# Kernel optimization log

Hardware: AMD Instinct MI355X
Metric: run time of the kernel (lower is better)

## Reference

```python
import jax, jax.numpy as jnp
import numpy as np

N = 4096
IN_DIM, HID, OUT_DIM = 512, 256, 64
PROP_STEP = 10
LAM_HAT = 0.9
SCAD_A = 3.7
EPS = 1e-8


def setup_inputs() -> dict:
    key = jax.random.key(0)
    kA, kF, k1, k2 = jax.random.split(key, 4)
    # sparse symmetric 0/1 adjacency, zero diagonal (add_loops adds I later)
    u = jax.random.uniform(kA, (N, N), dtype=jnp.float32)
    A = (u < 0.005).astype(jnp.float32)
    A = jnp.maximum(A, A.T)
    A = A * (1.0 - jnp.eye(N, dtype=jnp.float32))
    F = jax.random.normal(kF, (N, IN_DIM), dtype=jnp.float32)
    W1 = jax.random.normal(k1, (IN_DIM, HID), dtype=jnp.float32) / np.sqrt(IN_DIM)
    b1 = jnp.zeros((HID,), dtype=jnp.float32)
    W2 = jax.random.normal(k2, (HID, OUT_DIM), dtype=jnp.float32) / np.sqrt(HID)
    b2 = jnp.zeros((OUT_DIM,), dtype=jnp.float32)
    raw_gamma = jnp.zeros((PROP_STEP,), dtype=jnp.float32)
    return {"A": A, "F": F, "W1": W1, "b1": b1, "W2": W2, "b2": b2,
            "raw_gamma": raw_gamma}


def reference(A, F, W1, b1, W2, b2, raw_gamma):
    lam = 1.0 / LAM_HAT - 1.0
    a = SCAD_A
    # MLP (dropout inactive at inference)
    F0 = jax.nn.relu(F @ W1 + b1) @ W2 + b2            # [N, out_dim]
    eye = jnp.eye(A.shape[0], dtype=A.dtype)
    A = A + eye                                        # add_loops
    D = A.sum(-1)                                      # [N]
    D_sq = jnp.sqrt(D)[:, None]                        # [N, 1]
    A_tilde = A / D_sq / D_sq.T                        # sym_norm: D^-1/2 A D^-1/2
    gammas = jax.nn.sigmoid(raw_gamma) * 2.0           # per-layer gamma in (0, 2)

    def step(Fc, gamma_k):
        Fn = Fc / D_sq
        nrm = jnp.linalg.norm(Fn, axis=-1, keepdims=True)
        Fu = Fn / jnp.maximum(nrm, 1e-12)
        # cosine distance in [0, 2]; detached as in torch (.detach())
        y = jax.lax.stop_gradient(1.0 - Fu @ Fu.T)     # [N, N]
        lam_k = jnp.maximum(gamma_k / a, EPS)
        t = a * lam_k
        safe_y = jnp.where(y <= 0.0, 1.0, y)
        w_mid = (t - y) / ((a - 1.0) * safe_y)
        # SCAD weight: 1 for y<=lam_k, linear decay on [lam_k, a*lam_k], 0 beyond
        W = jnp.where(y <= lam_k, 1.0, jnp.where(y <= t, w_mid, 0.0))
        W = W * (1.0 - eye)
        W = jnp.where(jnp.isnan(W), 1.0, W)
        Q_hat = ((W * A).sum(-1) / D + lam)[:, None]   # [N, 1]
        F_new = (W * A_tilde) @ Fc / Q_hat + lam * F0 / Q_hat
        return F_new, None

    F_out, _ = jax.lax.scan(step, F0, gammas)
    return F_out
```

## Files before the change

kernel.cpp:

```cpp
#include <hip/hip_runtime.h>
#include <hip/hip_bf16.h>

#define N_NODES 4096
#define IN_DIM  512
#define HID_DIM 256
#define OUT_DIM 64
#define PROP_STEP 10
#define MAX_DEG 128
#define KSPLIT  4
#define MLP1_BLOCKS (64 * 4 * KSPLIT)
#define LAM_CONST (1.0f/0.9f - 1.0f)
#define SCAD_A 3.7f

__device__ __forceinline__ ushort f2bf(float f) {
    unsigned u = __float_as_uint(f);
    unsigned r = (u + 0x7FFFu + ((u >> 16) & 1u)) >> 16;
    return (ushort)r;
}
__device__ __forceinline__ unsigned pack2(float lo, float hi) {
    return (unsigned)f2bf(lo) | ((unsigned)f2bf(hi) << 16);
}
__device__ __forceinline__ float bflo(unsigned u) { return __uint_as_float(u << 16); }
__device__ __forceinline__ float bfhi(unsigned u) { return __uint_as_float(u & 0xFFFF0000u); }

__device__ __forceinline__ float wave_reduce_add(float v) {
#pragma unroll
    for (int off = 32; off > 0; off >>= 1) v += __shfl_xor(v, off, 64);
    return v;
}

__global__ __launch_bounds__(256) void build_mlp1(
    const float* __restrict__ A, const float* __restrict__ F,
    const float* __restrict__ W1, float* __restrict__ Hp,
    int* __restrict__ ell, int* __restrict__ deg,
    float* __restrict__ invD, float* __restrict__ invDsq)
{
    if (blockIdx.x < MLP1_BLOCKS) {
        __shared__ float sA[16][68];
        __shared__ float sB[16][68];
        int bid = blockIdx.x;
        int t  = threadIdx.x;
        int m0 = (bid & 63) * 64;
        int n0 = ((bid >> 6) & 3) * 64;
        int kp = bid >> 8;
        int tm = (t & 15) * 4;
        int tn = (t >> 4) * 4;
        int ar = t >> 2;
        int ac = (t & 3) * 4;
        int br = t >> 4;
        int bc = (t & 15) * 4;
        float acc[4][4] = {};
        int k0 = kp * (IN_DIM / KSPLIT);
        for (int kc = k0; kc < k0 + IN_DIM / KSPLIT; kc += 16) {
            float4 va = *(const float4*)(F  + (size_t)(m0 + ar) * IN_DIM + kc + ac);
            float4 vb = *(const float4*)(W1 + (size_t)(kc + br) * HID_DIM + n0 + bc);
            __syncthreads();
            sA[ac + 0][ar] = va.x;
            sA[ac + 1][ar] = va.y;
            sA[ac + 2][ar] = va.z;
            sA[ac + 3][ar] = va.w;
            *(float4*)&sB[br][bc] = vb;
            __syncthreads();
#pragma unroll
            for (int k = 0; k < 16; k++) {
                float4 a = *(const float4*)&sA[k][tm];
                float4 b = *(const float4*)&sB[k][tn];
                acc[0][0] += a.x * b.x; acc[0][1] += a.x * b.y; acc[0][2] += a.x * b.z; acc[0][3] += a.x * b.w;
                acc[1][0] += a.y * b.x; acc[1][1] += a.y * b.y; acc[1][2] += a.y * b.z; acc[1][3] += a.y * b.w;
                acc[2][0] += a.z * b.x; acc[2][1] += a.z * b.y; acc[2][2] += a.z * b.z; acc[2][3] += a.z * b.w;
                acc[3][0] += a.w * b.x; acc[3][1] += a.w * b.y; acc[3][2] += a.w * b.z; acc[3][3] += a.w * b.w;
            }
        }
        float* Hb = Hp + (size_t)kp * N_NODES * HID_DIM;
#pragma unroll
        for (int r = 0; r < 4; r++) {
            *(float4*)&Hb[(size_t)(m0 + tm + r) * HID_DIM + n0 + tn] =
                make_float4(acc[r][0], acc[r][1], acc[r][2], acc[r][3]);
        }
    } else {
        __shared__ int cnt;
        int i = blockIdx.x - MLP1_BLOCKS;
        int t = threadIdx.x;
        if (t == 0) cnt = 0;
        __syncthreads();
        const float4* row = (const float4*)(A + (size_t)i * N_NODES);
        for (int q = t; q < N_NODES / 4; q += 256) {
            float4 v = row[q];
            if (v.x != 0.0f) { int p = atomicAdd(&cnt, 1); if (p < MAX_DEG) ell[i * MAX_DEG + p] = q * 4 + 0; }
            if (v.y != 0.0f) { int p = atomicAdd(&cnt, 1); if (p < MAX_DEG) ell[i * MAX_DEG + p] = q * 4 + 1; }
            if (v.z != 0.0f) { int p = atomicAdd(&cnt, 1); if (p < MAX_DEG) ell[i * MAX_DEG + p] = q * 4 + 2; }
            if (v.w != 0.0f) { int p = atomicAdd(&cnt, 1); if (p < MAX_DEG) ell[i * MAX_DEG + p] = q * 4 + 3; }
        }
        __syncthreads();
        if (t == 0) {
            int c = cnt;
            if (c > MAX_DEG) c = MAX_DEG;
            deg[i] = c;
            int pad = (c + 15) & ~15;
            if (pad > MAX_DEG) pad = MAX_DEG;
            for (int p = c; p < pad; p++) ell[i * MAX_DEG + p] = i;
            float d = (float)(cnt + 1);
            invD[i] = 1.0f / d;
            invDsq[i] = rsqrtf(d);
        }
    }
}

__global__ __launch_bounds__(256) void mlp2r(
    const float* __restrict__ Hp, const float* __restrict__ b1,
    const float* __restrict__ W2, const float* __restrict__ b2,
    const float* __restrict__ invDsq,
    float* __restrict__ F0, unsigned* __restrict__ P0, float* __restrict__ nrm0)
{
    __shared__ float sW2[HID_DIM * OUT_DIM];
    __shared__ float hbuf[4][HID_DIM];
    int tid  = threadIdx.x;
    int wid  = tid >> 6, lane = tid & 63;
    int row  = blockIdx.x * 4 + wid;
    const size_t PS = (size_t)N_NODES * HID_DIM;

    for (int i = tid; i < HID_DIM * OUT_DIM / 4; i += 256)
        ((float4*)sW2)[i] = ((const float4*)W2)[i];

    const float* hrow = Hp + (size_t)row * HID_DIM + lane * 4;
    float4 s0 = *(const float4*)(hrow);
    float4 s1 = *(const float4*)(hrow + PS);
    float4 s2 = *(const float4*)(hrow + 2 * PS);
    float4 s3 = *(const float4*)(hrow + 3 * PS);
    float4 bb = *(const float4*)(b1 + lane * 4);
    float h0 = fmaxf(s0.x + s1.x + s2.x + s3.x + bb.x, 0.0f);
    float h1 = fmaxf(s0.y + s1.y + s2.y + s3.y + bb.y, 0.0f);
    float h2 = fmaxf(s0.z + s1.z + s2.z + s3.z + bb.z, 0.0f);
    float h3 = fmaxf(s0.w + s1.w + s2.w + s3.w + bb.w, 0.0f);
    __syncthreads();
    hbuf[wid][lane * 4 + 0] = h0;
    hbuf[wid][lane * 4 + 1] = h1;
    hbuf[wid][lane * 4 + 2] = h2;
    hbuf[wid][lane * 4 + 3] = h3;
    __syncthreads();

    float acc = b2[lane];
#pragma unroll 8
    for (int k = 0; k < HID_DIM; k++) {
        acc += hbuf[wid][k] * sW2[k * OUT_DIM + lane];
    }

    size_t o = (size_t)row * OUT_DIM + lane;
    F0[o] = acc;
    float fn = acc * invDsq[row];
    float nrm = fmaxf(sqrtf(wave_reduce_add(fn * fn)), 1e-12f);
    float fu = fn / nrm;
    float fu_hi = __shfl_xor(fu, 1, 64);
    if ((lane & 1) == 0) {
        P0[(size_t)row * 32 + (lane >> 1)] = pack2(fu, fu_hi);
    }
    if (lane == 0) nrm0[row] = nrm;
}

__global__ __launch_bounds__(256, 4) void propagate(
    const unsigned* __restrict__ Pin, const float* __restrict__ nrmIn,
    const float* __restrict__ F0,
    const int* __restrict__ ell, const int* __restrict__ deg,
    const float* __restrict__ invD, const float* __restrict__ invDsq,
    const float* __restrict__ raw_gamma, int step,
    unsigned* __restrict__ Pout, float* __restrict__ nrmOut,
    float* __restrict__ FcOut, int writeNext, int writeOut)
{
    int lane = threadIdx.x & 63;
    int wid  = threadIdx.x >> 6;
    int r    = __builtin_amdgcn_readfirstlane(blockIdx.x * 4 + wid);
    int g    = lane >> 3;
    int sl   = lane & 7;
    const float inv_am1 = 1.0f / (SCAD_A - 1.0f);

    float gamma = 2.0f / (1.0f + expf(-raw_gamma[step]));
    float lam_k = fmaxf(gamma / SCAD_A, 1e-8f);
    float tt    = SCAD_A * lam_k;

    int dg = deg[r];
    int pad = (dg + 15) & ~15;
    int npair = pad >> 4;
    const int* nb = ell + (size_t)r * MAX_DEG;
    int ed0 = (lane < pad)      ? nb[lane]      : r;
    int ed1 = (64 + lane < pad) ? nb[64 + lane] : r;

    uint4 up = *(const uint4*)(Pin + (size_t)r * 32 + sl * 4);
    float ui[8] = { bflo(up.x), bfhi(up.x), bflo(up.y), bfhi(up.y),
                    bflo(up.z), bfhi(up.z), bflo(up.w), bfhi(up.w) };

    float acc[8] = {};
    float qsum = 0.0f;
    for (int it = 0; it < npair; ++it) {
        int e0 = it * 16 + g;
        int e1 = e0 + 8;
        int src = (it < 4) ? ed0 : ed1;
        int j0 = __shfl(src, e0 & 63, 64);
        int j1 = __shfl(src, e1 & 63, 64);
        uint4 u0 = *(const uint4*)(Pin + (size_t)j0 * 32 + sl * 4);
        uint4 u1 = *(const uint4*)(Pin + (size_t)j1 * 32 + sl * 4);
        float nr0 = nrmIn[j0];
        float nr1 = nrmIn[j1];

        float pa = ui[0] * bflo(u0.x) + ui[1] * bfhi(u0.x) + ui[2] * bflo(u0.y) + ui[3] * bfhi(u0.y)
                 + ui[4] * bflo(u0.z) + ui[5] * bfhi(u0.z) + ui[6] * bflo(u0.w) + ui[7] * bfhi(u0.w);
        float pb = ui[0] * bflo(u1.x) + ui[1] * bfhi(u1.x) + ui[2] * bflo(u1.y) + ui[3] * bfhi(u1.y)
                 + ui[4] * bflo(u1.z) + ui[5] * bfhi(u1.z) + ui[6] * bflo(u1.w) + ui[7] * bfhi(u1.w);
        pa += __shfl_xor(pa, 1, 64); pb += __shfl_xor(pb, 1, 64);
        pa += __shfl_xor(pa, 2, 64); pb += __shfl_xor(pb, 2, 64);
        pa += __shfl_xor(pa, 4, 64); pb += __shfl_xor(pb, 4, 64);
        float ya = 1.0f - pa, yb = 1.0f - pb;
        float wa = (ya <= lam_k) ? 1.0f : ((ya <= tt) ? (tt - ya) * inv_am1 / ya : 0.0f);
        float wb = (yb <= lam_k) ? 1.0f : ((yb <= tt) ? (tt - yb) * inv_am1 / yb : 0.0f);
        if (e0 >= dg) wa = 0.0f;
        if (e1 >= dg) wb = 0.0f;
        qsum += wa + wb;
        float wsa = wa * nr0;
        float wsb = wb * nr1;
        acc[0] += wsa * bflo(u0.x) + wsb * bflo(u1.x);
        acc[1] += wsa * bfhi(u0.x) + wsb * bfhi(u1.x);
        acc[2] += wsa * bflo(u0.y) + wsb * bflo(u1.y);
        acc[3] += wsa * bfhi(u0.y) + wsb * bfhi(u1.y);
        acc[4] += wsa * bflo(u0.z) + wsb * bflo(u1.z);
        acc[5] += wsa * bfhi(u0.z) + wsb * bfhi(u1.z);
        acc[6] += wsa * bflo(u0.w) + wsb * bflo(u1.w);
        acc[7] += wsa * bfhi(u0.w) + wsb * bfhi(u1.w);
    }

#pragma unroll
    for (int off = 8; off <= 32; off <<= 1) {
#pragma unroll
        for (int q = 0; q < 8; q++) acc[q] += __shfl_xor(acc[q], off, 64);
        qsum += __shfl_xor(qsum, off, 64);
    }

    float iDs = invDsq[r];
    float Qh  = qsum * invD[r] + LAM_CONST;
    float rQh = 1.0f / Qh;
    const float4* f04 = (const float4*)(F0 + (size_t)r * OUT_DIM + sl * 8);
    float4 f0a = f04[0], f0b = f04[1];
    float f0v[8] = { f0a.x, f0a.y, f0a.z, f0a.w, f0b.x, f0b.y, f0b.z, f0b.w };
    float res[8];
#pragma unroll
    for (int q = 0; q < 8; q++) res[q] = (acc[q] * iDs + LAM_CONST * f0v[q]) * rQh;

    if (writeOut && lane < 8) {
        float4* o4 = (float4*)(FcOut + (size_t)r * OUT_DIM + sl * 8);
        o4[0] = make_float4(res[0], res[1], res[2], res[3]);
        o4[1] = make_float4(res[4], res[5], res[6], res[7]);
    }
    if (writeNext) {
        float fn[8];
        float ssq = 0.0f;
#pragma unroll
        for (int q = 0; q < 8; q++) { fn[q] = res[q] * iDs; ssq += fn[q] * fn[q]; }
        ssq += __shfl_xor(ssq, 1, 64);
        ssq += __shfl_xor(ssq, 2, 64);
        ssq += __shfl_xor(ssq, 4, 64);
        float nrm = fmaxf(sqrtf(ssq), 1e-12f);
        float inv_n = 1.0f / nrm;
        if (lane < 8) {
            uint4 fuPk;
            fuPk.x = pack2(fn[0] * inv_n, fn[1] * inv_n);
            fuPk.y = pack2(fn[2] * inv_n, fn[3] * inv_n);
            fuPk.z = pack2(fn[4] * inv_n, fn[5] * inv_n);
            fuPk.w = pack2(fn[6] * inv_n, fn[7] * inv_n);
            *(uint4*)(Pout + (size_t)r * 32 + sl * 4) = fuPk;
        }
        if (lane == 0) nrmOut[r] = nrm;
    }
}

extern "C" void kernel_launch(void* const* d_in, const int* in_sizes, int n_in,
                              void* d_out, int out_size, void* d_ws, size_t ws_size,
                              hipStream_t stream)
{
    const float* A  = (const float*)d_in[0];
    const float* F  = (const float*)d_in[1];
    const float* W1 = (const float*)d_in[2];
    const float* b1 = (const float*)d_in[3];
    const float* W2 = (const float*)d_in[4];
    const float* b2 = (const float*)d_in[5];
    const float* rg = (const float*)d_in[6];
    float* out = (float*)d_out;

    char* p = (char*)d_ws;
    float* Hp     = (float*)p; p += (size_t)KSPLIT * N_NODES * HID_DIM * 4;
    float* F0     = (float*)p; p += (size_t)N_NODES * OUT_DIM * 4;
    unsigned* Pa  = (unsigned*)p; p += (size_t)N_NODES * 32 * 4;
    unsigned* Pb  = (unsigned*)p; p += (size_t)N_NODES * 32 * 4;
    float* nrmA   = (float*)p; p += (size_t)N_NODES * 4;
    float* nrmB   = (float*)p; p += (size_t)N_NODES * 4;
    float* invD   = (float*)p; p += (size_t)N_NODES * 4;
    float* invDsq = (float*)p; p += (size_t)N_NODES * 4;
    int*   deg    = (int*)p;   p += (size_t)N_NODES * 4;
    int*   ell    = (int*)p;   p += (size_t)N_NODES * MAX_DEG * 4;

    build_mlp1<<<MLP1_BLOCKS + N_NODES, 256, 0, stream>>>(
        A, F, W1, Hp, ell, deg, invD, invDsq);
    mlp2r<<<N_NODES / 4, 256, 0, stream>>>(Hp, b1, W2, b2, invDsq, F0, Pa, nrmA);

    for (int k = 0; k < PROP_STEP; k++) {
        unsigned* Pin   = (k & 1) ? Pb : Pa;
        unsigned* Pout  = (k & 1) ? Pa : Pb;
        float* nIn      = (k & 1) ? nrmB : nrmA;
        float* nOut     = (k & 1) ? nrmA : nrmB;
        int last = (k == PROP_STEP - 1);
        propagate<<<N_NODES / 4, 256, 0, stream>>>(
            Pin, nIn, F0, ell, deg, invD, invDsq, rg, k,
            Pout, nOut, out, !last, last);
    }
}
```

Before: 207.7 us.

## Fuse full MLP into build kernel, fold first step, software-pipeline neighbor loads

Fuses both MLP layers into one GEMM path per 16-row block, removing the split-K partial buffer and the separate mlp2r kernel. Folds the initial normalization into a specialized first propagation step that reads F0 directly. Adds double-buffered prefetch of neighbor rows in the propagate loop to hide gather latency. The trade-off is fewer GEMM blocks (256) with more work each, which may reduce parallelism for the first layer.

```diff
diff --git a/kernel.cpp b/kernel.cpp
--- a/kernel.cpp
+++ b/kernel.cpp
@@ -7,8 +7,7 @@
 #define OUT_DIM 64
 #define PROP_STEP 10
 #define MAX_DEG 128
-#define KSPLIT  4
-#define MLP1_BLOCKS (64 * 4 * KSPLIT)
+#define GEMM_BLOCKS 256
 #define LAM_CONST (1.0f/0.9f - 1.0f)
 #define SCAD_A 3.7f
 
@@ -23,68 +22,80 @@
 __device__ __forceinline__ float bflo(unsigned u) { return __uint_as_float(u << 16); }
 __device__ __forceinline__ float bfhi(unsigned u) { return __uint_as_float(u & 0xFFFF0000u); }
 
-__device__ __forceinline__ float wave_reduce_add(float v) {
-#pragma unroll
-    for (int off = 32; off > 0; off >>= 1) v += __shfl_xor(v, off, 64);
-    return v;
-}
-
-__global__ __launch_bounds__(256) void build_mlp1(
+__global__ __launch_bounds__(512) void build_all(
     const float* __restrict__ A, const float* __restrict__ F,
-    const float* __restrict__ W1, float* __restrict__ Hp,
+    const float* __restrict__ W1, const float* __restrict__ b1,
+    const float* __restrict__ W2, const float* __restrict__ b2,
+    float* __restrict__ F0,
     int* __restrict__ ell, int* __restrict__ deg,
     float* __restrict__ invD, float* __restrict__ invDsq)
 {
-    if (blockIdx.x < MLP1_BLOCKS) {
-        __shared__ float sA[16][68];
-        __shared__ float sB[16][68];
-        int bid = blockIdx.x;
+    if (blockIdx.x < GEMM_BLOCKS) {
+        __shared__ float sFt[16][20];
+        __shared__ float sW[16][272];
+        __shared__ float sH[16][260];
         int t  = threadIdx.x;
-        int m0 = (bid & 63) * 64;
-        int n0 = ((bid >> 6) & 3) * 64;
-        int kp = bid >> 8;
-        int tm = (t & 15) * 4;
-        int tn = (t >> 4) * 4;
-        int ar = t >> 2;
-        int ac = (t & 3) * 4;
-        int br = t >> 4;
-        int bc = (t & 15) * 4;
-        float acc[4][4] = {};
-        int k0 = kp * (IN_DIM / KSPLIT);
-        for (int kc = k0; kc < k0 + IN_DIM / KSPLIT; kc += 16) {
-            float4 va = *(const float4*)(F  + (size_t)(m0 + ar) * IN_DIM + kc + ac);
-            float4 vb = *(const float4*)(W1 + (size_t)(kc + br) * HID_DIM + n0 + bc);
+        int m0 = blockIdx.x * 16;
+        int tm = (t & 7) * 2;
+        int tn = (t >> 3) * 4;
+        int fr = t >> 4, fk = t & 15;
+        int wr = t >> 6, wc = (t & 63) * 4;
+        float a00 = 0.f, a01 = 0.f, a02 = 0.f, a03 = 0.f;
+        float a10 = 0.f, a11 = 0.f, a12 = 0.f, a13 = 0.f;
+        for (int kc = 0; kc < IN_DIM; kc += 16) {
+            float fv = 0.0f;
+            if (t < 256) fv = F[(size_t)(m0 + fr) * IN_DIM + kc + fk];
+            float4 w0 = *(const float4*)(W1 + (size_t)(kc + wr)     * HID_DIM + wc);
+            float4 w1 = *(const float4*)(W1 + (size_t)(kc + 8 + wr) * HID_DIM + wc);
             __syncthreads();
-            sA[ac + 0][ar] = va.x;
-            sA[ac + 1][ar] = va.y;
-            sA[ac + 2][ar] = va.z;
-            sA[ac + 3][ar] = va.w;
-            *(float4*)&sB[br][bc] = vb;
+            if (t < 256) sFt[fk][fr] = fv;
+            *(float4*)&sW[wr][wc]     = w0;
+            *(float4*)&sW[8 + wr][wc] = w1;
             __syncthreads();
 #pragma unroll
             for (int k = 0; k < 16; k++) {
-                float4 a = *(const float4*)&sA[k][tm];
-                float4 b = *(const float4*)&sB[k][tn];
-                acc[0][0] += a.x * b.x; acc[0][1] += a.x * b.y; acc[0][2] += a.x * b.z; acc[0][3] += a.x * b.w;
-                acc[1][0] += a.y * b.x; acc[1][1] += a.y * b.y; acc[1][2] += a.y * b.z; acc[1][3] += a.y * b.w;
-                acc[2][0] += a.z * b.x; acc[2][1] += a.z * b.y; acc[2][2] += a.z * b.z; acc[2][3] += a.z * b.w;
-                acc[3][0] += a.w * b.x; acc[3][1] += a.w * b.y; acc[3][2] += a.w * b.z; acc[3][3] += a.w * b.w;
+                float2 a = *(const float2*)&sFt[k][tm];
+                float4 b = *(const float4*)&sW[k][tn];
+                a00 += a.x * b.x; a01 += a.x * b.y; a02 += a.x * b.z; a03 += a.x * b.w;
+                a10 += a.y * b.x; a11 += a.y * b.y; a12 += a.y * b.z; a13 += a.y * b.w;
             }
         }
-        float* Hb = Hp + (size_t)kp * N_NODES * HID_DIM;
-#pragma unroll
-        for (int r = 0; r < 4; r++) {
-            *(float4*)&Hb[(size_t)(m0 + tm + r) * HID_DIM + n0 + tn] =
-                make_float4(acc[r][0], acc[r][1], acc[r][2], acc[r][3]);
-        }
+        float4 bb = *(const float4*)(b1 + tn);
+        *(float4*)&sH[tm][tn] = make_float4(
+            fmaxf(a00 + bb.x, 0.f), fmaxf(a01 + bb.y, 0.f),
+            fmaxf(a02 + bb.z, 0.f), fmaxf(a03 + bb.w, 0.f));
+        *(float4*)&sH[tm + 1][tn] = make_float4(
+            fmaxf(a10 + bb.x, 0.f), fmaxf(a11 + bb.y, 0.f),
+            fmaxf(a12 + bb.z, 0.f), fmaxf(a13 + bb.w, 0.f));
+        __syncthreads();
+        int r2 = t >> 5;
+        int c2 = (t & 31) * 2;
+        float accA = b2[c2], accB = b2[c2 + 1];
+        float (*sW2c)[68] = (float(*)[68])sW;
+        for (int kc = 0; kc < HID_DIM; kc += 64) {
+            __syncthreads();
+            for (int i = t; i < 1024; i += 512) {
+                int kk = i >> 4, cc = (i & 15) * 4;
+                *(float4*)&sW2c[kk][cc] =
+                    *(const float4*)(W2 + (size_t)(kc + kk) * OUT_DIM + cc);
+            }
+            __syncthreads();
+#pragma unroll 8
+            for (int k = 0; k < 64; k++) {
+                float  hb = sH[r2][kc + k];
+                float2 w2 = *(const float2*)&sW2c[k][c2];
+                accA += hb * w2.x; accB += hb * w2.y;
+            }
+        }
+        *(float2*)(F0 + (size_t)(m0 + r2) * OUT_DIM + c2) = make_float2(accA, accB);
     } else {
         __shared__ int cnt;
-        int i = blockIdx.x - MLP1_BLOCKS;
+        int i = blockIdx.x - GEMM_BLOCKS;
         int t = threadIdx.x;
         if (t == 0) cnt = 0;
         __syncthreads();
         const float4* row = (const float4*)(A + (size_t)i * N_NODES);
-        for (int q = t; q < N_NODES / 4; q += 256) {
+        for (int q = t; q < N_NODES / 4; q += 512) {
             float4 v = row[q];
             if (v.x != 0.0f) { int p = atomicAdd(&cnt, 1); if (p < MAX_DEG) ell[i * MAX_DEG + p] = q * 4 + 0; }
             if (v.y != 0.0f) { int p = atomicAdd(&cnt, 1); if (p < MAX_DEG) ell[i * MAX_DEG + p] = q * 4 + 1; }
@@ -106,55 +117,115 @@
     }
 }
 
-__global__ __launch_bounds__(256) void mlp2r(
-    const float* __restrict__ Hp, const float* __restrict__ b1,
-    const float* __restrict__ W2, const float* __restrict__ b2,
-    const float* __restrict__ invDsq,
-    float* __restrict__ F0, unsigned* __restrict__ P0, float* __restrict__ nrm0)
+__global__ __launch_bounds__(256, 4) void propagate_f0(
+    const float* __restrict__ F0,
+    const int* __restrict__ ell, const int* __restrict__ deg,
+    const float* __restrict__ invD, const float* __restrict__ invDsq,
+    const float* __restrict__ raw_gamma,
+    unsigned* __restrict__ Pout, float* __restrict__ nrmOut)
 {
-    __shared__ float sW2[HID_DIM * OUT_DIM];
-    __shared__ float hbuf[4][HID_DIM];
-    int tid  = threadIdx.x;
-    int wid  = tid >> 6, lane = tid & 63;
-    int row  = blockIdx.x * 4 + wid;
-    const size_t PS = (size_t)N_NODES * HID_DIM;
-
-    for (int i = tid; i < HID_DIM * OUT_DIM / 4; i += 256)
-        ((float4*)sW2)[i] = ((const float4*)W2)[i];
-
-    const float* hrow = Hp + (size_t)row * HID_DIM + lane * 4;
-    float4 s0 = *(const float4*)(hrow);
-    float4 s1 = *(const float4*)(hrow + PS);
-    float4 s2 = *(const float4*)(hrow + 2 * PS);
-    float4 s3 = *(const float4*)(hrow + 3 * PS);
-    float4 bb = *(const float4*)(b1 + lane * 4);
-    float h0 = fmaxf(s0.x + s1.x + s2.x + s3.x + bb.x, 0.0f);
-    float h1 = fmaxf(s0.y + s1.y + s2.y + s3.y + bb.y, 0.0f);
-    float h2 = fmaxf(s0.z + s1.z + s2.z + s3.z + bb.z, 0.0f);
-    float h3 = fmaxf(s0.w + s1.w + s2.w + s3.w + bb.w, 0.0f);
-    __syncthreads();
-    hbuf[wid][lane * 4 + 0] = h0;
-    hbuf[wid][lane * 4 + 1] = h1;
-    hbuf[wid][lane * 4 + 2] = h2;
-    hbuf[wid][lane * 4 + 3] = h3;
-    __syncthreads();
-
-    float acc = b2[lane];
-#pragma unroll 8
-    for (int k = 0; k < HID_DIM; k++) {
-        acc += hbuf[wid][k] * sW2[k * OUT_DIM + lane];
-    }
-
-    size_t o = (size_t)row * OUT_DIM + lane;
-    F0[o] = acc;
-    float fn = acc * invDsq[row];
-    float nrm = fmaxf(sqrtf(wave_reduce_add(fn * fn)), 1e-12f);
-    float fu = fn / nrm;
-    float fu_hi = __shfl_xor(fu, 1, 64);
-    if ((lane & 1) == 0) {
-        P0[(size_t)row * 32 + (lane >> 1)] = pack2(fu, fu_hi);
-    }
-    if (lane == 0) nrm0[row] = nrm;
+    int lane = threadIdx.x & 63;
+    int wid  = threadIdx.x >> 6;
+    int r    = __builtin_amdgcn_readfirstlane(blockIdx.x * 4 + wid);
+    int g    = lane >> 3;
+    int sl   = lane & 7;
+    const float inv_am1 = 1.0f / (SCAD_A - 1.0f);
+
+    float gamma = 2.0f / (1.0f + expf(-raw_gamma[0]));
+    float lam_k = fmaxf(gamma / SCAD_A, 1e-8f);
+    float tt    = SCAD_A * lam_k;
+
+    int dg = deg[r];
+    int pad = (dg + 15) & ~15;
+    int npair = pad >> 4;
+    const int* nb = ell + (size_t)r * MAX_DEG;
+    int ed0 = (lane < pad)      ? nb[lane]      : r;
+    int ed1 = (64 + lane < pad) ? nb[64 + lane] : r;
+
+    float iDs = invDsq[r];
+    const float4* f04 = (const float4*)(F0 + (size_t)r * OUT_DIM + sl * 8);
+    float4 fa = f04[0], fb = f04[1];
+    float f0v[8] = { fa.x, fa.y, fa.z, fa.w, fb.x, fb.y, fb.z, fb.w };
+    float ui[8];
+    float ssr = 0.0f;
+#pragma unroll
+    for (int q = 0; q < 8; q++) { ui[q] = f0v[q] * iDs; ssr += ui[q] * ui[q]; }
+    ssr += __shfl_xor(ssr, 1, 64);
+    ssr += __shfl_xor(ssr, 2, 64);
+    ssr += __shfl_xor(ssr, 4, 64);
+    float inv_nr = 1.0f / fmaxf(sqrtf(ssr), 1e-12f);
+#pragma unroll
+    for (int q = 0; q < 8; q++) ui[q] *= inv_nr;
+
+    float acc[8] = {};
+    float qsum = 0.0f;
+    for (int it = 0; it < npair; ++it) {
+        int e0 = it * 16 + g, e1 = e0 + 8;
+        int src = (it < 4) ? ed0 : ed1;
+        int j0 = __shfl(src, e0 & 63, 64);
+        int j1 = __shfl(src, e1 & 63, 64);
+        const float4* p0 = (const float4*)(F0 + (size_t)j0 * OUT_DIM + sl * 8);
+        const float4* p1 = (const float4*)(F0 + (size_t)j1 * OUT_DIM + sl * 8);
+        float4 x0 = p0[0], x1 = p0[1];
+        float4 y0 = p1[0], y1 = p1[1];
+        float d0 = invDsq[j0], d1 = invDsq[j1];
+        float v0[8] = { x0.x*d0, x0.y*d0, x0.z*d0, x0.w*d0, x1.x*d0, x1.y*d0, x1.z*d0, x1.w*d0 };
+        float v1[8] = { y0.x*d1, y0.y*d1, y0.z*d1, y0.w*d1, y1.x*d1, y1.y*d1, y1.z*d1, y1.w*d1 };
+        float pa = 0.f, pb = 0.f, s0 = 0.f, s1 = 0.f;
+#pragma unroll
+        for (int q = 0; q < 8; q++) {
+            pa += ui[q] * v0[q]; s0 += v0[q] * v0[q];
+            pb += ui[q] * v1[q]; s1 += v1[q] * v1[q];
+        }
+        pa += __shfl_xor(pa, 1, 64); pb += __shfl_xor(pb, 1, 64);
+        s0 += __shfl_xor(s0, 1, 64); s1 += __shfl_xor(s1, 1, 64);
+        pa += __shfl_xor(pa, 2, 64); pb += __shfl_xor(pb, 2, 64);
+        s0 += __shfl_xor(s0, 2, 64); s1 += __shfl_xor(s1, 2, 64);
+        pa += __shfl_xor(pa, 4, 64); pb += __shfl_xor(pb, 4, 64);
+        s0 += __shfl_xor(s0, 4, 64); s1 += __shfl_xor(s1, 4, 64);
+        float n0 = fmaxf(sqrtf(s0), 1e-12f);
+        float n1 = fmaxf(sqrtf(s1), 1e-12f);
+        float ya = 1.0f - pa / n0, yb = 1.0f - pb / n1;
+        float wa = (ya <= lam_k) ? 1.0f : ((ya <= tt) ? (tt - ya) * inv_am1 / ya : 0.0f);
+        float wb = (yb <= lam_k) ? 1.0f : ((yb <= tt) ? (tt - yb) * inv_am1 / yb : 0.0f);
+        if (e0 >= dg) wa = 0.0f;
+        if (e1 >= dg) wb = 0.0f;
+        qsum += wa + wb;
+#pragma unroll
+        for (int q = 0; q < 8; q++) acc[q] += wa * v0[q] + wb * v1[q];
+    }
+
+#pragma unroll
+    for (int off = 8; off <= 32; off <<= 1) {
+#pragma unroll
+        for (int q = 0; q < 8; q++) acc[q] += __shfl_xor(acc[q], off, 64);
+        qsum += __shfl_xor(qsum, off, 64);
+    }
+
+    float Qh  = qsum * invD[r] + LAM_CONST;
+    float rQh = 1.0f / Qh;
+    float res[8], fn[8];
+    float ssq = 0.0f;
+#pragma unroll
+    for (int q = 0; q < 8; q++) {
+        res[q] = (acc[q] * iDs + LAM_CONST * f0v[q]) * rQh;
+        fn[q]  = res[q] * iDs;
+        ssq   += fn[q] * fn[q];
+    }
+    ssq += __shfl_xor(ssq, 1, 64);
+    ssq += __shfl_xor(ssq, 2, 64);
+    ssq += __shfl_xor(ssq, 4, 64);
+    float nrm = fmaxf(sqrtf(ssq), 1e-12f);
+    float inv_n = 1.0f / nrm;
+    if (lane < 8) {
+        uint4 fuPk;
+        fuPk.x = pack2(fn[0] * inv_n, fn[1] * inv_n);
+        fuPk.y = pack2(fn[2] * inv_n, fn[3] * inv_n);
+        fuPk.z = pack2(fn[4] * inv_n, fn[5] * inv_n);
+        fuPk.w = pack2(fn[6] * inv_n, fn[7] * inv_n);
+        *(uint4*)(Pout + (size_t)r * 32 + sl * 4) = fuPk;
+    }
+    if (lane == 0) nrmOut[r] = nrm;
 }
 
 __global__ __launch_bounds__(256, 4) void propagate(
@@ -190,40 +261,67 @@
 
     float acc[8] = {};
     float qsum = 0.0f;
-    for (int it = 0; it < npair; ++it) {
-        int e0 = it * 16 + g;
-        int e1 = e0 + 8;
-        int src = (it < 4) ? ed0 : ed1;
-        int j0 = __shfl(src, e0 & 63, 64);
-        int j1 = __shfl(src, e1 & 63, 64);
-        uint4 u0 = *(const uint4*)(Pin + (size_t)j0 * 32 + sl * 4);
-        uint4 u1 = *(const uint4*)(Pin + (size_t)j1 * 32 + sl * 4);
-        float nr0 = nrmIn[j0];
-        float nr1 = nrmIn[j1];
-
-        float pa = ui[0] * bflo(u0.x) + ui[1] * bfhi(u0.x) + ui[2] * bflo(u0.y) + ui[3] * bfhi(u0.y)
-                 + ui[4] * bflo(u0.z) + ui[5] * bfhi(u0.z) + ui[6] * bflo(u0.w) + ui[7] * bfhi(u0.w);
-        float pb = ui[0] * bflo(u1.x) + ui[1] * bfhi(u1.x) + ui[2] * bflo(u1.y) + ui[3] * bfhi(u1.y)
-                 + ui[4] * bflo(u1.z) + ui[5] * bfhi(u1.z) + ui[6] * bflo(u1.w) + ui[7] * bfhi(u1.w);
+
+    auto eidx = [&](int it_, int& J0, int& J1) {
+        int e0_ = it_ * 16 + g;
+        int src = (it_ < 4) ? ed0 : ed1;
+        J0 = __shfl(src, e0_ & 63, 64);
+        J1 = __shfl(src, (e0_ + 8) & 63, 64);
+    };
+    auto body = [&](int it_, uint4 U0, uint4 U1, float NR0, float NR1) {
+        float pa = ui[0] * bflo(U0.x) + ui[1] * bfhi(U0.x) + ui[2] * bflo(U0.y) + ui[3] * bfhi(U0.y)
+                 + ui[4] * bflo(U0.z) + ui[5] * bfhi(U0.z) + ui[6] * bflo(U0.w) + ui[7] * bfhi(U0.w);
+        float pb = ui[0] * bflo(U1.x) + ui[1] * bfhi(U1.x) + ui[2] * bflo(U1.y) + ui[3] * bfhi(U1.y)
+                 + ui[4] * bflo(U1.z) + ui[5] * bfhi(U1.z) + ui[6] * bflo(U1.w) + ui[7] * bfhi(U1.w);
         pa += __shfl_xor(pa, 1, 64); pb += __shfl_xor(pb, 1, 64);
         pa += __shfl_xor(pa, 2, 64); pb += __shfl_xor(pb, 2, 64);
         pa += __shfl_xor(pa, 4, 64); pb += __shfl_xor(pb, 4, 64);
         float ya = 1.0f - pa, yb = 1.0f - pb;
         float wa = (ya <= lam_k) ? 1.0f : ((ya <= tt) ? (tt - ya) * inv_am1 / ya : 0.0f);
         float wb = (yb <= lam_k) ? 1.0f : ((yb <= tt) ? (tt - yb) * inv_am1 / yb : 0.0f);
-        if (e0 >= dg) wa = 0.0f;
-        if (e1 >= dg) wb = 0.0f;
+        int e0_ = it_ * 16 + g;
+        if (e0_ >= dg)     wa = 0.0f;
+        if (e0_ + 8 >= dg) wb = 0.0f;
         qsum += wa + wb;
-        float wsa = wa * nr0;
-        float wsb = wb * nr1;
-        acc[0] += wsa * bflo(u0.x) + wsb * bflo(u1.x);
-        acc[1] += wsa * bfhi(u0.x) + wsb * bfhi(u1.x);
-        acc[2] += wsa * bflo(u0.y) + wsb * bflo(u1.y);
-        acc[3] += wsa * bfhi(u0.y) + wsb * bfhi(u1.y);
-        acc[4] += wsa * bflo(u0.z) + wsb * bflo(u1.z);
-        acc[5] += wsa * bfhi(u0.z) + wsb * bfhi(u1.z);
-        acc[6] += wsa * bflo(u0.w) + wsb * bflo(u1.w);
-        acc[7] += wsa * bfhi(u0.w) + wsb * bfhi(u1.w);
+        float wsa = wa * NR0;
+        float wsb = wb * NR1;
+        acc[0] += wsa * bflo(U0.x) + wsb * bflo(U1.x);
+        acc[1] += wsa * bfhi(U0.x) + wsb * bfhi(U1.x);
+        acc[2] += wsa * bflo(U0.y) + wsb * bflo(U1.y);
+        acc[3] += wsa * bfhi(U0.y) + wsb * bfhi(U1.y);
+        acc[4] += wsa * bflo(U0.z) + wsb * bflo(U1.z);
+        acc[5] += wsa * bfhi(U0.z) + wsb * bfhi(U1.z);
+        acc[6] += wsa * bflo(U0.w) + wsb * bflo(U1.w);
+        acc[7] += wsa * bfhi(U0.w) + wsb * bfhi(U1.w);
+    };
+
+    if (npair > 0) {
+        uint4 uA0, uA1, uB0, uB1;
+        float nA0, nA1, nB0, nB1;
+        int j0, j1;
+        eidx(0, j0, j1);
+        uA0 = *(const uint4*)(Pin + (size_t)j0 * 32 + sl * 4);
+        uA1 = *(const uint4*)(Pin + (size_t)j1 * 32 + sl * 4);
+        nA0 = nrmIn[j0]; nA1 = nrmIn[j1];
+        int it = 0;
+        while (true) {
+            if (it + 1 < npair) {
+                eidx(it + 1, j0, j1);
+                uB0 = *(const uint4*)(Pin + (size_t)j0 * 32 + sl * 4);
+                uB1 = *(const uint4*)(Pin + (size_t)j1 * 32 + sl * 4);
+                nB0 = nrmIn[j0]; nB1 = nrmIn[j1];
+            }
+            body(it, uA0, uA1, nA0, nA1);
+            ++it; if (it >= npair) break;
+            if (it + 1 < npair) {
+                eidx(it + 1, j0, j1);
+                uA0 = *(const uint4*)(Pin + (size_t)j0 * 32 + sl * 4);
+                uA1 = *(const uint4*)(Pin + (size_t)j1 * 32 + sl * 4);
+                nA0 = nrmIn[j0]; nA1 = nrmIn[j1];
+            }
+            body(it, uB0, uB1, nB0, nB1);
+            ++it; if (it >= npair) break;
+        }
     }
 
 #pragma unroll
@@ -284,7 +382,6 @@
     float* out = (float*)d_out;
 
     char* p = (char*)d_ws;
-    float* Hp     = (float*)p; p += (size_t)KSPLIT * N_NODES * HID_DIM * 4;
     float* F0     = (float*)p; p += (size_t)N_NODES * OUT_DIM * 4;
     unsigned* Pa  = (unsigned*)p; p += (size_t)N_NODES * 32 * 4;
     unsigned* Pb  = (unsigned*)p; p += (size_t)N_NODES * 32 * 4;
@@ -295,15 +392,17 @@
     int*   deg    = (int*)p;   p += (size_t)N_NODES * 4;
     int*   ell    = (int*)p;   p += (size_t)N_NODES * MAX_DEG * 4;
 
-    build_mlp1<<<MLP1_BLOCKS + N_NODES, 256, 0, stream>>>(
-        A, F, W1, Hp, ell, deg, invD, invDsq);
-    mlp2r<<<N_NODES / 4, 256, 0, stream>>>(Hp, b1, W2, b2, invDsq, F0, Pa, nrmA);
-
-    for (int k = 0; k < PROP_STEP; k++) {
-        unsigned* Pin   = (k & 1) ? Pb : Pa;
-        unsigned* Pout  = (k & 1) ? Pa : Pb;
-        float* nIn      = (k & 1) ? nrmB : nrmA;
-        float* nOut     = (k & 1) ? nrmA : nrmB;
+    build_all<<<GEMM_BLOCKS + N_NODES, 512, 0, stream>>>(
+        A, F, W1, b1, W2, b2, F0, ell, deg, invD, invDsq);
+
+    propagate_f0<<<N_NODES / 4, 256, 0, stream>>>(
+        F0, ell, deg, invD, invDsq, rg, Pa, nrmA);
+
+    for (int k = 1; k < PROP_STEP; k++) {
+        unsigned* Pin   = (k & 1) ? Pa : Pb;
+        unsigned* Pout  = (k & 1) ? Pb : Pa;
+        float* nIn      = (k & 1) ? nrmA : nrmB;
+        float* nOut     = (k & 1) ? nrmB : nrmA;
         int last = (k == PROP_STEP - 1);
         propagate<<<N_NODES / 4, 256, 0, stream>>>(
             Pin, nIn, F0, ell, deg, invD, invDsq, rg, k,
```

Result: no change. 209.7 us (+1.0%).
